# Kernel optimization log

Hardware: AMD Instinct MI355X
Metric: run time of the kernel (lower is better)

Reference implementation:

```python
import jax, jax.numpy as jnp
import numpy as np

DIM = 1024
N_HEAD = 16
HEAD_DIM = DIM // N_HEAD
HIDDEN = 4 * DIM
EPS = 1e-6
NEG = -1e9


def setup_inputs() -> dict:
    key = jax.random.key(0)
    ks = jax.random.split(key, 9)
    B, T = 2, 2048
    x = jax.random.normal(ks[0], (B, T, DIM), dtype=jnp.float32)
    # additive causal mask [T, T]
    mask = jnp.where(jnp.tril(jnp.ones((T, T), dtype=bool)), 0.0, NEG).astype(jnp.float32)
    s = 0.02
    wq = jax.random.normal(ks[1], (DIM, DIM), dtype=jnp.float32) * s
    wk = jax.random.normal(ks[2], (DIM, DIM), dtype=jnp.float32) * s
    wv = jax.random.normal(ks[3], (DIM, DIM), dtype=jnp.float32) * s
    wo = jax.random.normal(ks[4], (DIM, DIM), dtype=jnp.float32) * s
    w1 = jax.random.normal(ks[5], (DIM, HIDDEN), dtype=jnp.float32) * s
    w2 = jax.random.normal(ks[6], (HIDDEN, DIM), dtype=jnp.float32) * s
    g_attn = jnp.ones((DIM,), dtype=jnp.float32)
    g_ffn = jnp.ones((DIM,), dtype=jnp.float32)
    return {"x": x, "mask": mask, "wq": wq, "wk": wk, "wv": wv, "wo": wo,
            "w1": w1, "w2": w2, "g_attn": g_attn, "g_ffn": g_ffn}


def _rmsnorm(x, g):
    norm = jax.lax.rsqrt(jnp.mean(jnp.square(x), axis=-1, keepdims=True) + EPS)
    return (x * norm) * g


def _attention(x, mask, wq, wk, wv, wo):
    B, T, C = x.shape
    # project and split heads: [B, H, T, D]
    q = (x @ wq).reshape(B, T, N_HEAD, HEAD_DIM).transpose(0, 2, 1, 3)
    k = (x @ wk).reshape(B, T, N_HEAD, HEAD_DIM).transpose(0, 2, 1, 3)
    v = (x @ wv).reshape(B, T, N_HEAD, HEAD_DIM).transpose(0, 2, 1, 3)
    attn = jnp.einsum('bhtd,bhsd->bhts', q, k) / np.sqrt(HEAD_DIM).astype(np.float32)
    attn = attn + mask  # broadcast [T,T] over [B,H,T,T]
    p = jax.nn.softmax(attn, axis=-1)
    out = jnp.einsum('bhts,bhsd->bhtd', p, v)
    out = out.transpose(0, 2, 1, 3).reshape(B, T, C)
    return out @ wo


def reference(x, mask, wq, wk, wv, wo, w1, w2, g_attn, g_ffn):
    x = x + _attention(_rmsnorm(x, g_attn), mask, wq, wk, wv, wo)
    h = _rmsnorm(x, g_ffn)
    return x + (jax.nn.silu(h @ w1) @ w2)
```

## Files before the change

kernel.cpp:

```cpp
#include <hip/hip_runtime.h>
#include <hip/hip_bf16.h>
#include <cstdint>
#include <cstddef>

#define DIM    1024
#define NHEAD  16
#define HDIM   64
#define HIDDEN 4096
#define TSEQ   2048
#define TOKENS 4096

typedef __attribute__((ext_vector_type(4))) float  f32x4;
typedef __attribute__((ext_vector_type(8))) short  short8;
typedef __attribute__((ext_vector_type(8))) __bf16 bf16x8;

__device__ __forceinline__ short f2bf(float f) {
    union { float f; uint32_t u; } v; v.f = f;
    uint32_t u = v.u;
    uint32_t r = (u + 0x7fffu + ((u >> 16) & 1u)) >> 16;
    return (short)r;
}

__device__ __forceinline__ f32x4 mfma_bf16(short8 a, short8 b, f32x4 c) {
    return __builtin_amdgcn_mfma_f32_16x16x32_bf16(
        __builtin_bit_cast(bf16x8, a), __builtin_bit_cast(bf16x8, b), c, 0, 0, 0);
}

__global__ __launch_bounds__(256) void transpose_w(
    const float* __restrict__ W, short* __restrict__ Wt, int K, int N)
{
    __shared__ float tile[64][65];
    const int tid = threadIdx.x;
    const int n0 = blockIdx.x * 64, k0 = blockIdx.y * 64;
    for (int i = tid; i < 4096; i += 256) {
        int r = i >> 6, c = i & 63;
        tile[r][c] = W[(size_t)(k0 + r) * N + n0 + c];
    }
    __syncthreads();
    for (int i = tid; i < 4096; i += 256) {
        int r = i >> 6, c = i & 63;
        Wt[(size_t)(n0 + r) * K + k0 + c] = f2bf(tile[c][r]);
    }
}

__global__ __launch_bounds__(256) void transpose_v(
    const short* __restrict__ qkv, short* __restrict__ Vt)
{
    __shared__ short tile[64][72];
    const int tid = threadIdx.x;
    const int s0 = blockIdx.x * 64, bh = blockIdx.y;
    const int b = bh >> 4, h = bh & 15;
    const short* src = qkv + ((size_t)(b * TSEQ + s0)) * 3072 + 2048 + h * 64;
    for (int i = tid; i < 512; i += 256) {
        int r = i >> 3, cg = i & 7;
        *(short8*)&tile[r][cg * 8] = *(const short8*)(src + (size_t)r * 3072 + cg * 8);
    }
    __syncthreads();
    short* dst = Vt + ((size_t)bh * 64) * TSEQ + s0;
    for (int i = tid; i < 512; i += 256) {
        int d = i >> 3, sg = i & 7;
        short8 o;
#pragma unroll
        for (int j = 0; j < 8; ++j) o[j] = tile[sg * 8 + j][d];
        *(short8*)(dst + (size_t)d * TSEQ + sg * 8) = o;
    }
}

__global__ __launch_bounds__(256) void rmsnorm_k(
    const float* __restrict__ x, const float* __restrict__ g, short* __restrict__ out)
{
    const int t = blockIdx.x, tid = threadIdx.x;
    const int wave = tid >> 6, lane = tid & 63;
    const float4 v = ((const float4*)(x + (size_t)t * DIM))[tid];
    float ss = v.x * v.x + v.y * v.y + v.z * v.z + v.w * v.w;
#pragma unroll
    for (int d = 1; d < 64; d <<= 1) ss += __shfl_xor(ss, d, 64);
    __shared__ float red[4];
    if (lane == 0) red[wave] = ss;
    __syncthreads();
    float tot = red[0] + red[1] + red[2] + red[3];
    float rn = rsqrtf(tot * (1.0f / (float)DIM) + 1e-6f);
    const float4 gv = ((const float4*)g)[tid];
    short4 ov = make_short4(f2bf(v.x * rn * gv.x), f2bf(v.y * rn * gv.y),
                            f2bf(v.z * rn * gv.z), f2bf(v.w * rn * gv.w));
    ((short4*)(out + (size_t)t * DIM))[tid] = ov;
}

template <int EPI>
__global__ __launch_bounds__(256) void gemm_bt(
    const short* __restrict__ A, const short* __restrict__ Bt,
    void* __restrict__ Cout, const float* __restrict__ res,
    int M, int N, int K)
{
    __shared__ short As[128 * 32];
    __shared__ short Bs[128 * 32];
    const int tid  = threadIdx.x;
    const int wave = tid >> 6, lane = tid & 63;
    const int lm = lane & 15, quad = lane >> 4;
    const int wm = wave & 1, wn = wave >> 1;
    const int m0 = blockIdx.y * 128, n0 = blockIdx.x * 128;
    const int Ksl = K / gridDim.z;
    const int kbeg = blockIdx.z * Ksl, kend = kbeg + Ksl;

    const f32x4 zero = {0.f, 0.f, 0.f, 0.f};
    f32x4 acc[4][4];
#pragma unroll
    for (int i = 0; i < 4; ++i)
#pragma unroll
        for (int j = 0; j < 4; ++j) acc[i][j] = zero;

    const int lrow = wave * 32 + (lane >> 2);
    const int lcol = (lane & 3) * 8;
    const short* Ap = A + (size_t)(m0 + lrow) * K + kbeg + lcol;
    const short* Bp = Bt + (size_t)(n0 + lrow) * K + kbeg + lcol;
    short* Asw = &As[lrow * 32 + lcol];
    short* Bsw = &Bs[lrow * 32 + lcol];

    short8 ga0, ga1, gb0, gb1;
    ga0 = *(const short8*)Ap;
    ga1 = *(const short8*)(Ap + (size_t)16 * K);
    gb0 = *(const short8*)Bp;
    gb1 = *(const short8*)(Bp + (size_t)16 * K);
    Ap += 32; Bp += 32;

    for (int k0 = kbeg; k0 < kend; k0 += 32) {
        __syncthreads();
        *(short8*)Asw = ga0;
        *(short8*)(Asw + 16 * 32) = ga1;
        *(short8*)Bsw = gb0;
        *(short8*)(Bsw + 16 * 32) = gb1;
        __syncthreads();
        if (k0 + 32 < kend) {
            ga0 = *(const short8*)Ap;
            ga1 = *(const short8*)(Ap + (size_t)16 * K);
            gb0 = *(const short8*)Bp;
            gb1 = *(const short8*)(Bp + (size_t)16 * K);
            Ap += 32; Bp += 32;
        }
        short8 af[4], bf[4];
#pragma unroll
        for (int mt = 0; mt < 4; ++mt)
            af[mt] = *(const short8*)&As[(wm * 64 + mt * 16 + lm) * 32 + quad * 8];
#pragma unroll
        for (int nt = 0; nt < 4; ++nt)
            bf[nt] = *(const short8*)&Bs[(wn * 64 + nt * 16 + lm) * 32 + quad * 8];
#pragma unroll
        for (int mt = 0; mt < 4; ++mt)
#pragma unroll
            for (int nt = 0; nt < 4; ++nt)
                acc[mt][nt] = mfma_bf16(af[mt], bf[nt], acc[mt][nt]);
    }

#pragma unroll
    for (int mt = 0; mt < 4; ++mt) {
#pragma unroll
        for (int r = 0; r < 4; ++r) {
            const int row = m0 + wm * 64 + mt * 16 + quad * 4 + r;
#pragma unroll
            for (int nt = 0; nt < 4; ++nt) {
                const int col = n0 + wn * 64 + nt * 16 + lm;
                const size_t idx = (size_t)row * N + col;
                const float v = acc[mt][nt][r];
                if constexpr (EPI == 0) {
                    ((short*)Cout)[idx] = f2bf(v);
                } else if constexpr (EPI == 1) {
                    ((float*)Cout)[idx] = res[idx] + v;
                } else if constexpr (EPI == 2) {
                    ((short*)Cout)[idx] = f2bf(v / (1.0f + __expf(-v)));
                } else {
                    ((float*)Cout)[(size_t)blockIdx.z * M * N + idx] = v;
                }
            }
        }
    }
}

__global__ __launch_bounds__(256) void combine_k(
    const float* __restrict__ p, const float* __restrict__ res,
    float* __restrict__ out, int n)
{
    const int i = blockIdx.x * 256 + threadIdx.x;
    if (i * 4 < n) {
        float4 a = ((const float4*)res)[i];
        float4 b = ((const float4*)p)[i];
        float4 c = ((const float4*)(p + n))[i];
        float4 o = make_float4(a.x + b.x + c.x, a.y + b.y + c.y,
                               a.z + b.z + c.z, a.w + b.w + c.w);
        ((float4*)out)[i] = o;
    }
}

#define LP 72
__global__ __launch_bounds__(128) void attn_k(
    const short* __restrict__ qkv, const short* __restrict__ Vt,
    short* __restrict__ out)
{
    __shared__ short Qs[64 * LP];
    __shared__ short Ks[64 * LP];
    __shared__ short Vts[64 * LP];
    __shared__ short Ps[2][32 * LP];

    const int tid = threadIdx.x, wave = tid >> 6, lane = tid & 63;
    const int lm = lane & 15, quad = lane >> 4;
    const int bh = blockIdx.x;
    const int qt = (gridDim.y - 1) - blockIdx.y;
    const int b = bh >> 4, h = bh & 15;
    const int q0 = qt * 64;

    const int rr = tid >> 3, cg = tid & 7;

    const short* qbase = qkv + ((size_t)(b * TSEQ + q0)) * 3072 + h * 64;
#pragma unroll
    for (int j = 0; j < 4; ++j)
        *(short8*)&Qs[(rr + j * 16) * LP + cg * 8] =
            *(const short8*)(qbase + (size_t)(rr + j * 16) * 3072 + cg * 8);

    const short* kb  = qkv + (size_t)b * TSEQ * 3072 + 1024 + h * 64;
    const short* vtb = Vt + (size_t)bh * 64 * TSEQ;

    short8 kr[4], vr[4];
#pragma unroll
    for (int j = 0; j < 4; ++j) {
        kr[j] = *(const short8*)(kb + (size_t)(rr + j * 16) * 3072 + cg * 8);
        vr[j] = *(const short8*)(vtb + (size_t)(rr + j * 16) * TSEQ + cg * 8);
    }

    const f32x4 zero = {0.f, 0.f, 0.f, 0.f};
    f32x4 o_acc[2][4];
#pragma unroll
    for (int mt = 0; mt < 2; ++mt)
#pragma unroll
        for (int t = 0; t < 4; ++t) o_acc[mt][t] = zero;
    float lsum[2][4] = {{0.f, 0.f, 0.f, 0.f}, {0.f, 0.f, 0.f, 0.f}};

    for (int st = 0; st <= qt; ++st) {
        __syncthreads();
#pragma unroll
        for (int j = 0; j < 4; ++j) {
            *(short8*)&Ks[(rr + j * 16) * LP + cg * 8] = kr[j];
            *(short8*)&Vts[(rr + j * 16) * LP + cg * 8] = vr[j];
        }
        __syncthreads();
        if (st < qt) {
            const size_t sn = (size_t)(st + 1) * 64;
#pragma unroll
            for (int j = 0; j < 4; ++j) {
                kr[j] = *(const short8*)(kb + (sn + rr + j * 16) * 3072 + cg * 8);
                vr[j] = *(const short8*)(vtb + (size_t)(rr + j * 16) * TSEQ + sn + cg * 8);
            }
        }

        f32x4 sa[2][4];
#pragma unroll
        for (int mt = 0; mt < 2; ++mt)
#pragma unroll
            for (int nt = 0; nt < 4; ++nt) sa[mt][nt] = zero;
#pragma unroll
        for (int kk = 0; kk < 2; ++kk) {
            short8 aq0 = *(const short8*)&Qs[(wave * 32 + lm) * LP + kk * 32 + quad * 8];
            short8 aq1 = *(const short8*)&Qs[(wave * 32 + 16 + lm) * LP + kk * 32 + quad * 8];
#pragma unroll
            for (int nt = 0; nt < 4; ++nt) {
                short8 bk = *(const short8*)&Ks[(nt * 16 + lm) * LP + kk * 32 + quad * 8];
                sa[0][nt] = mfma_bf16(aq0, bk, sa[0][nt]);
                sa[1][nt] = mfma_bf16(aq1, bk, sa[1][nt]);
            }
        }

        const int s0 = st * 64;
        const bool band = (st == qt);
#pragma unroll
        for (int mt = 0; mt < 2; ++mt) {
            const int qrow = q0 + wave * 32 + mt * 16 + quad * 4;
#pragma unroll
            for (int nt = 0; nt < 4; ++nt) {
                const int col = s0 + nt * 16 + lm;
#pragma unroll
                for (int r = 0; r < 4; ++r) {
                    float p = __expf(0.125f * sa[mt][nt][r]);
                    if (band && col > qrow + r) p = 0.f;
                    lsum[mt][r] += p;
                    Ps[wave][(mt * 16 + quad * 4 + r) * LP + nt * 16 + lm] =
                        (short)(__builtin_bit_cast(uint32_t, p) >> 16);
                }
            }
        }

#pragma unroll
        for (int kk = 0; kk < 2; ++kk) {
            short8 ap0 = *(const short8*)&Ps[wave][lm * LP + kk * 32 + quad * 8];
            short8 ap1 = *(const short8*)&Ps[wave][(16 + lm) * LP + kk * 32 + quad * 8];
#pragma unroll
            for (int t = 0; t < 4; ++t) {
                short8 bv = *(const short8*)&Vts[(t * 16 + lm) * LP + kk * 32 + quad * 8];
                o_acc[0][t] = mfma_bf16(ap0, bv, o_acc[0][t]);
                o_acc[1][t] = mfma_bf16(ap1, bv, o_acc[1][t]);
            }
        }
    }

#pragma unroll
    for (int mt = 0; mt < 2; ++mt)
#pragma unroll
        for (int r = 0; r < 4; ++r) {
            float s = lsum[mt][r];
#pragma unroll
            for (int d = 1; d < 16; d <<= 1) s += __shfl_xor(s, d, 16);
            lsum[mt][r] = s;
        }

#pragma unroll
    for (int mt = 0; mt < 2; ++mt)
#pragma unroll
        for (int r = 0; r < 4; ++r) {
            const float inv = 1.0f / lsum[mt][r];
            const int token = b * TSEQ + q0 + wave * 32 + mt * 16 + quad * 4 + r;
#pragma unroll
            for (int t = 0; t < 4; ++t)
                out[(size_t)token * 1024 + h * 64 + t * 16 + lm] = f2bf(o_acc[mt][t][r] * inv);
        }
}

extern "C" void kernel_launch(void* const* d_in, const int* in_sizes, int n_in,
                              void* d_out, int out_size, void* d_ws, size_t ws_size,
                              hipStream_t stream)
{
    const float* x      = (const float*)d_in[0];
    const float* wq     = (const float*)d_in[2];
    const float* wk     = (const float*)d_in[3];
    const float* wv     = (const float*)d_in[4];
    const float* wo     = (const float*)d_in[5];
    const float* w1     = (const float*)d_in[6];
    const float* w2     = (const float*)d_in[7];
    const float* g_attn = (const float*)d_in[8];
    const float* g_ffn  = (const float*)d_in[9];
    float* out = (float*)d_out;

    char* ws = (char*)d_ws;
    const size_t MB = 1024 * 1024;
    short* Wqkv_t = (short*)(ws + 0);
    short* Wo_t   = (short*)(ws + 6 * MB);
    short* W1_t   = (short*)(ws + 8 * MB);
    short* xn     = (short*)(ws + 16 * MB);
    short* hbuf   = (short*)(ws + 24 * MB);
    short* qkv    = (short*)(ws + 32 * MB);
    float* pbufO  = (float*)(ws + 32 * MB);
    short* Vt     = (short*)(ws + 64 * MB);
    float* x2     = (float*)(ws + 64 * MB);
    short* W2_t   = (short*)(ws + 80 * MB);
    float* pbuf2  = (float*)(ws + 0);

    dim3 blk(256);

    transpose_w<<<dim3(16, 16), blk, 0, stream>>>(wq, Wqkv_t, 1024, 1024);
    transpose_w<<<dim3(16, 16), blk, 0, stream>>>(wk, Wqkv_t + (size_t)1024 * 1024, 1024, 1024);
    transpose_w<<<dim3(16, 16), blk, 0, stream>>>(wv, Wqkv_t + (size_t)2048 * 1024, 1024, 1024);
    transpose_w<<<dim3(16, 16), blk, 0, stream>>>(wo, Wo_t, 1024, 1024);
    transpose_w<<<dim3(64, 16), blk, 0, stream>>>(w1, W1_t, 1024, 4096);
    transpose_w<<<dim3(16, 64), blk, 0, stream>>>(w2, W2_t, 4096, 1024);

    rmsnorm_k<<<TOKENS, blk, 0, stream>>>(x, g_attn, xn);

    gemm_bt<0><<<dim3(3072 / 128, TOKENS / 128), blk, 0, stream>>>(
        xn, Wqkv_t, qkv, nullptr, TOKENS, 3072, 1024);

    transpose_v<<<dim3(TSEQ / 64, 32), blk, 0, stream>>>(qkv, Vt);

    attn_k<<<dim3(32, TSEQ / 64), dim3(128), 0, stream>>>(qkv, Vt, xn);

    gemm_bt<3><<<dim3(1024 / 128, TOKENS / 128, 2), blk, 0, stream>>>(
        xn, Wo_t, pbufO, nullptr, TOKENS, 1024, 1024);
    combine_k<<<dim3(TOKENS * DIM / 4 / 256), blk, 0, stream>>>(
        pbufO, x, x2, TOKENS * DIM);

    rmsnorm_k<<<TOKENS, blk, 0, stream>>>(x2, g_ffn, hbuf);

    gemm_bt<2><<<dim3(HIDDEN / 128, TOKENS / 128), blk, 0, stream>>>(
        hbuf, W1_t, qkv, nullptr, TOKENS, HIDDEN, 1024);

    gemm_bt<3><<<dim3(1024 / 128, TOKENS / 128, 2), blk, 0, stream>>>(
        qkv, W2_t, pbuf2, nullptr, TOKENS, 1024, HIDDEN);

    combine_k<<<dim3(TOKENS * DIM / 4 / 256), blk, 0, stream>>>(
        pbuf2, x2, out, TOKENS * DIM);
}
```

Baseline: 379.6 us.

## Double-buffer GEMM shared-memory tiles and fuse split-K combine with RMSNorm

The GEMM now keeps two shared-memory buffers, so the store of the next K tile overlaps the MFMA work on the current one. This needs one barrier per iteration instead of two. A second change fuses the split-K combine of the output projection with the FFN RMSNorm into one kernel, which removes a launch and a re-read of x2. The cost is doubled LDS per block (32KB), which may lower occupancy.

```diff
diff --git a/kernel.cpp b/kernel.cpp
--- a/kernel.cpp
+++ b/kernel.cpp
@@ -92,15 +92,16 @@
     void* __restrict__ Cout, const float* __restrict__ res,
     int M, int N, int K)
 {
-    __shared__ short As[128 * 32];
-    __shared__ short Bs[128 * 32];
+    __shared__ short As[2][128 * 32];
+    __shared__ short Bs[2][128 * 32];
     const int tid  = threadIdx.x;
     const int wave = tid >> 6, lane = tid & 63;
     const int lm = lane & 15, quad = lane >> 4;
     const int wm = wave & 1, wn = wave >> 1;
     const int m0 = blockIdx.y * 128, n0 = blockIdx.x * 128;
     const int Ksl = K / gridDim.z;
-    const int kbeg = blockIdx.z * Ksl, kend = kbeg + Ksl;
+    const int kbeg = blockIdx.z * Ksl;
+    const int nIter = Ksl >> 5;
 
     const f32x4 zero = {0.f, 0.f, 0.f, 0.f};
     f32x4 acc[4][4];
@@ -113,8 +114,7 @@
     const int lcol = (lane & 3) * 8;
     const short* Ap = A + (size_t)(m0 + lrow) * K + kbeg + lcol;
     const short* Bp = Bt + (size_t)(n0 + lrow) * K + kbeg + lcol;
-    short* Asw = &As[lrow * 32 + lcol];
-    short* Bsw = &Bs[lrow * 32 + lcol];
+    const int woff = lrow * 32 + lcol;
 
     short8 ga0, ga1, gb0, gb1;
     ga0 = *(const short8*)Ap;
@@ -122,33 +122,51 @@
     gb0 = *(const short8*)Bp;
     gb1 = *(const short8*)(Bp + (size_t)16 * K);
     Ap += 32; Bp += 32;
-
-    for (int k0 = kbeg; k0 < kend; k0 += 32) {
-        __syncthreads();
-        *(short8*)Asw = ga0;
-        *(short8*)(Asw + 16 * 32) = ga1;
-        *(short8*)Bsw = gb0;
-        *(short8*)(Bsw + 16 * 32) = gb1;
-        __syncthreads();
-        if (k0 + 32 < kend) {
-            ga0 = *(const short8*)Ap;
-            ga1 = *(const short8*)(Ap + (size_t)16 * K);
-            gb0 = *(const short8*)Bp;
-            gb1 = *(const short8*)(Bp + (size_t)16 * K);
-            Ap += 32; Bp += 32;
-        }
+    *(short8*)&As[0][woff] = ga0;
+    *(short8*)&As[0][woff + 512] = ga1;
+    *(short8*)&Bs[0][woff] = gb0;
+    *(short8*)&Bs[0][woff + 512] = gb1;
+    if (nIter > 1) {
+        ga0 = *(const short8*)Ap;
+        ga1 = *(const short8*)(Ap + (size_t)16 * K);
+        gb0 = *(const short8*)Bp;
+        gb1 = *(const short8*)(Bp + (size_t)16 * K);
+        Ap += 32; Bp += 32;
+    }
+    __syncthreads();
+
+    for (int it = 0; it < nIter; ++it) {
+        const int cur = it & 1;
+        const short* as = As[cur];
+        const short* bs = Bs[cur];
         short8 af[4], bf[4];
 #pragma unroll
         for (int mt = 0; mt < 4; ++mt)
-            af[mt] = *(const short8*)&As[(wm * 64 + mt * 16 + lm) * 32 + quad * 8];
+            af[mt] = *(const short8*)&as[(wm * 64 + mt * 16 + lm) * 32 + quad * 8];
 #pragma unroll
         for (int nt = 0; nt < 4; ++nt)
-            bf[nt] = *(const short8*)&Bs[(wn * 64 + nt * 16 + lm) * 32 + quad * 8];
+            bf[nt] = *(const short8*)&bs[(wn * 64 + nt * 16 + lm) * 32 + quad * 8];
 #pragma unroll
         for (int mt = 0; mt < 4; ++mt)
 #pragma unroll
             for (int nt = 0; nt < 4; ++nt)
                 acc[mt][nt] = mfma_bf16(af[mt], bf[nt], acc[mt][nt]);
+
+        if (it + 1 < nIter) {
+            const int nxt = cur ^ 1;
+            *(short8*)&As[nxt][woff] = ga0;
+            *(short8*)&As[nxt][woff + 512] = ga1;
+            *(short8*)&Bs[nxt][woff] = gb0;
+            *(short8*)&Bs[nxt][woff + 512] = gb1;
+            if (it + 2 < nIter) {
+                ga0 = *(const short8*)Ap;
+                ga1 = *(const short8*)(Ap + (size_t)16 * K);
+                gb0 = *(const short8*)Bp;
+                gb1 = *(const short8*)(Bp + (size_t)16 * K);
+                Ap += 32; Bp += 32;
+            }
+        }
+        __syncthreads();
     }
 
 #pragma unroll
@@ -190,6 +208,34 @@
     }
 }
 
+__global__ __launch_bounds__(256) void combine_rms(
+    const float* __restrict__ p, const float* __restrict__ res,
+    const float* __restrict__ g, float* __restrict__ x2out,
+    short* __restrict__ nout)
+{
+    const int t = blockIdx.x, tid = threadIdx.x;
+    const int wave = tid >> 6, lane = tid & 63;
+    const size_t base = (size_t)t * DIM / 4;
+    float4 a = ((const float4*)res)[base + tid];
+    float4 b = ((const float4*)p)[base + tid];
+    float4 c = ((const float4*)p)[(size_t)TOKENS * DIM / 4 + base + tid];
+    float4 v = make_float4(a.x + b.x + c.x, a.y + b.y + c.y,
+                           a.z + b.z + c.z, a.w + b.w + c.w);
+    ((float4*)x2out)[base + tid] = v;
+    float ss = v.x * v.x + v.y * v.y + v.z * v.z + v.w * v.w;
+#pragma unroll
+    for (int d = 1; d < 64; d <<= 1) ss += __shfl_xor(ss, d, 64);
+    __shared__ float red[4];
+    if (lane == 0) red[wave] = ss;
+    __syncthreads();
+    float tot = red[0] + red[1] + red[2] + red[3];
+    float rn = rsqrtf(tot * (1.0f / (float)DIM) + 1e-6f);
+    const float4 gv = ((const float4*)g)[tid];
+    short4 ov = make_short4(f2bf(v.x * rn * gv.x), f2bf(v.y * rn * gv.y),
+                            f2bf(v.z * rn * gv.z), f2bf(v.w * rn * gv.w));
+    ((short4*)nout)[base + tid] = ov;
+}
+
 #define LP 72
 __global__ __launch_bounds__(128) void attn_k(
     const short* __restrict__ qkv, const short* __restrict__ Vt,
@@ -370,10 +416,8 @@
 
     gemm_bt<3><<<dim3(1024 / 128, TOKENS / 128, 2), blk, 0, stream>>>(
         xn, Wo_t, pbufO, nullptr, TOKENS, 1024, 1024);
-    combine_k<<<dim3(TOKENS * DIM / 4 / 256), blk, 0, stream>>>(
-        pbufO, x, x2, TOKENS * DIM);
-
-    rmsnorm_k<<<TOKENS, blk, 0, stream>>>(x2, g_ffn, hbuf);
+
+    combine_rms<<<TOKENS, blk, 0, stream>>>(pbufO, x, g_ffn, x2, hbuf);
 
     gemm_bt<2><<<dim3(HIDDEN / 128, TOKENS / 128), blk, 0, stream>>>(
         hbuf, W1_t, qkv, nullptr, TOKENS, HIDDEN, 1024);
```

Measured after the change: 394.8 us. 4.0% more time.
